# Performance work log

Measured on AMD Instinct MI355X. Metric: run time of the kernel, lower is better.

## Reference

```python
import jax, jax.numpy as jnp
import numpy as np

B, C, L = 8, 256, 2048
G = min(C // 4, 32)  # 32 groups
EPS = 1e-6


def group_norm(x, gamma, beta):
    # x: (B, C, L)
    xg = x.reshape(B, G, C // G, L)
    mean = xg.mean(axis=(2, 3), keepdims=True)
    var = xg.var(axis=(2, 3), keepdims=True)
    xn = ((xg - mean) * jax.lax.rsqrt(var + EPS)).reshape(B, C, L)
    return xn * gamma[None, :, None] + beta[None, :, None]


def nin(h, w, b):
    # 1x1 projection over channel dim: (B,C,L),(C,D)->(B,D,L)
    return jnp.einsum('bcl,cd->bdl', h, w) + b[None, :, None]


def setup_inputs() -> dict:
    key = jax.random.key(0)
    ks = jax.random.split(key, 10)
    s = 1.0 / np.sqrt(C)
    return {
        'x': jax.random.normal(ks[0], (B, C, L), dtype=jnp.float32),
        'gn_gamma': jnp.ones((C,), jnp.float32),
        'gn_beta': jnp.zeros((C,), jnp.float32),
        'w0': jax.random.normal(ks[1], (C, C), jnp.float32) * s,
        'b0': jnp.zeros((C,), jnp.float32),
        'w1': jax.random.normal(ks[2], (C, C), jnp.float32) * s,
        'b1': jnp.zeros((C,), jnp.float32),
        'w2': jax.random.normal(ks[3], (C, C), jnp.float32) * s,
        'b2': jnp.zeros((C,), jnp.float32),
        'w3': jax.random.normal(ks[4], (C, C), jnp.float32) * s,
        'b3': jnp.zeros((C,), jnp.float32),
    }


def reference(x, gn_gamma, gn_beta, w0, b0, w1, b1, w2, b2, w3, b3):
    h = group_norm(x, gn_gamma, gn_beta)
    q = nin(h, w0, b0)
    k = nin(h, w1, b1)
    v = nin(h, w2, b2)
    # attention scores over the L dim, scaled by 1/sqrt(C)
    w = jnp.einsum('bcl,bci->bli', q, k) * (C ** -0.5)  # (B, L, L)
    w = jax.nn.softmax(w, axis=-1)
    h = jnp.einsum('bli,bci->bcl', w, v)
    h = nin(h, w3, b3)
    return x + h  # skip_rescale=False
```

## Files before the change

### kernel.cpp

```cpp
#include <hip/hip_runtime.h>

#define B_ 8
#define C_ 256
#define L_ 2048
#define G_ 32
static constexpr long CL = (long)C_ * L_;
static constexpr long LL = (long)L_ * L_;

typedef __attribute__((ext_vector_type(8))) short bf16x8;
typedef __attribute__((ext_vector_type(4))) float f32x4;

__device__ __forceinline__ ushort f2bf(float f) {
    union { float f; unsigned u; } v; v.f = f;
    unsigned r = v.u + 0x7FFFu + ((v.u >> 16) & 1u);
    return (ushort)(r >> 16);
}
__device__ __forceinline__ float bf2f(ushort u) {
    union { unsigned u; float f; } v; v.u = (unsigned)u << 16;
    return v.f;
}

__device__ __forceinline__ void ld16(const ushort* g, ushort* l) {
    __builtin_amdgcn_global_load_lds(
        (const __attribute__((address_space(1))) unsigned int*)g,
        (__attribute__((address_space(3))) unsigned int*)l, 16, 0, 0);
}

__device__ __forceinline__ int swz8(int bid, int nwg) {
    return (bid & 7) * (nwg >> 3) + (bid >> 3);
}

template<int OP>
__device__ __forceinline__ float blockReduce(float v) {
    __shared__ float tmp[4];
    int lane = threadIdx.x & 63;
    int w    = threadIdx.x >> 6;
#pragma unroll
    for (int off = 32; off; off >>= 1) {
        float o = __shfl_down(v, off);
        v = OP ? fmaxf(v, o) : (v + o);
    }
    if (lane == 0) tmp[w] = v;
    __syncthreads();
    float r = OP ? fmaxf(fmaxf(tmp[0], tmp[1]), fmaxf(tmp[2], tmp[3]))
                 : (tmp[0] + tmp[1] + tmp[2] + tmp[3]);
    __syncthreads();
    return r;
}

__global__ __launch_bounds__(256) void gn_t_kernel(const float* __restrict__ x,
                                                   const float* __restrict__ gamma,
                                                   const float* __restrict__ beta,
                                                   ushort* __restrict__ hb) {
    int bg = blockIdx.x;
    int b  = bg >> 5, g = bg & 31;
    const float* xg = x + (long)bg * 16384;
    const float4* xv = (const float4*)xg;
    float s = 0.f, ss = 0.f;
    for (int i = threadIdx.x; i < 4096; i += 256) {
        float4 v = xv[i];
        s  += v.x + v.y + v.z + v.w;
        ss += v.x * v.x + v.y * v.y + v.z * v.z + v.w * v.w;
    }
    s  = blockReduce<0>(s);
    ss = blockReduce<0>(ss);
    float mean = s * (1.f / 16384.f);
    float var  = ss * (1.f / 16384.f) - mean * mean;
    float rstd = rsqrtf(var + 1e-6f);
    float a[8], bb[8];
#pragma unroll
    for (int cc = 0; cc < 8; ++cc) {
        int c = g * 8 + cc;
        a[cc]  = gamma[c] * rstd;
        bb[cc] = beta[c] - mean * a[cc];
    }
    ushort* hp = hb + (long)b * CL + g * 8;
    for (int l = threadIdx.x; l < 2048; l += 256) {
        ushort o[8];
#pragma unroll
        for (int cc = 0; cc < 8; ++cc)
            o[cc] = f2bf(xg[cc * 2048 + l] * a[cc] + bb[cc]);
        *(uint4*)&hp[(long)l * 256] = *(uint4*)o;
    }
}

__global__ void transpose_w(const float* __restrict__ w0, const float* __restrict__ w1,
                            const float* __restrict__ w2, const float* __restrict__ w3,
                            ushort* __restrict__ wT4) {
    int which = blockIdx.y;
    const float* w = which == 0 ? w0 : which == 1 ? w1 : which == 2 ? w2 : w3;
    int d = blockIdx.x, c = threadIdx.x;
    wT4[which * 65536 + d * 256 + c] = f2bf(w[c * 256 + d]);
}

template<int TM, int TN, int WR, int WC, bool DB>
__device__ __forceinline__ void gemm_body(const ushort* __restrict__ Mop,
                                          const ushort* __restrict__ Nop,
                                          long lda, long ldb, int K,
                                          ushort* As, ushort* Bs,
                                          f32x4 (&acc)[TM / (16 * WR)][TN / (16 * WC)]) {
    constexpr int NW = WR * WC;
    constexpr int CA = TM / (8 * NW), CB = TN / (8 * NW);
    constexpr int FM = TM / (16 * WR), FN = TN / (16 * WC);
    const int tid = threadIdx.x, lane = tid & 63, w = tid >> 6;
    const int r8 = lane >> 3, s8 = lane & 7;
    const int wrr = w / WC, wcc = w % WC;

    auto stage = [&](int buf, int k0) {
        ushort* Ad = As + buf * (TM * 64);
        ushort* Bd = Bs + buf * (TN * 64);
#pragma unroll
        for (int i = 0; i < CA; ++i) {
            int c = w * CA + i, row = c * 8 + r8;
            int ko = (s8 ^ (row & 7)) << 3;
            ld16(Mop + (long)row * lda + k0 + ko, Ad + c * 512);
        }
#pragma unroll
        for (int i = 0; i < CB; ++i) {
            int c = w * CB + i, row = c * 8 + r8;
            int ko = (s8 ^ (row & 7)) << 3;
            ld16(Nop + (long)row * ldb + k0 + ko, Bd + c * 512);
        }
    };

    auto compute = [&](int buf) {
        const ushort* Ac = As + buf * (TM * 64);
        const ushort* Bc = Bs + buf * (TN * 64);
#pragma unroll
        for (int kh = 0; kh < 2; ++kh) {
            int g = kh * 4 + (lane >> 4);
            bf16x8 av[FM], bv[FN];
#pragma unroll
            for (int mi = 0; mi < FM; ++mi) {
                int row = wrr * (TM / WR) + mi * 16 + (lane & 15);
                av[mi] = *(const bf16x8*)&Ac[row * 64 + ((g ^ (row & 7)) << 3)];
            }
#pragma unroll
            for (int ni = 0; ni < FN; ++ni) {
                int row = wcc * (TN / WC) + ni * 16 + (lane & 15);
                bv[ni] = *(const bf16x8*)&Bc[row * 64 + ((g ^ (row & 7)) << 3)];
            }
#pragma unroll
            for (int mi = 0; mi < FM; ++mi)
#pragma unroll
                for (int ni = 0; ni < FN; ++ni)
                    acc[mi][ni] = __builtin_amdgcn_mfma_f32_16x16x32_bf16(av[mi], bv[ni], acc[mi][ni], 0, 0, 0);
        }
    };

    if constexpr (!DB) {
        for (int k0 = 0; k0 < K; k0 += 64) {
            stage(0, k0);
            __syncthreads();
            compute(0);
            __syncthreads();
        }
    } else {
        stage(0, 0);
        asm volatile("s_waitcnt vmcnt(0)" ::: "memory");
        __builtin_amdgcn_s_barrier();
        int cur = 0;
        for (int k0 = 0; k0 < K; k0 += 64) {
            if (k0 + 64 < K) stage(cur ^ 1, k0 + 64);
            compute(cur);
            asm volatile("s_waitcnt vmcnt(0)" ::: "memory");
            __builtin_amdgcn_s_barrier();
            cur ^= 1;
        }
    }
}

#define GEMM_PROLOGUE(TM, TN, WR, WC, DBF)                    \
    __shared__ ushort As[DBF * TM * 64];                      \
    __shared__ ushort Bs[DBF * TN * 64];                      \
    f32x4 acc[TM / (16 * WR)][TN / (16 * WC)];                \
    _Pragma("unroll") for (int i = 0; i < TM / (16 * WR); ++i)     \
        _Pragma("unroll") for (int j = 0; j < TN / (16 * WC); ++j) \
            _Pragma("unroll") for (int e = 0; e < 4; ++e) acc[i][j][e] = 0.f; \
    const int lane = threadIdx.x & 63, wv = threadIdx.x >> 6; \
    const int wrr = wv / WC, wcc = wv % WC; (void)wrr; (void)wcc;

__global__ __launch_bounds__(256) void qkv_gemm(const ushort* __restrict__ wT4,
                                                const ushort* __restrict__ hb,
                                                ushort* __restrict__ qb,
                                                ushort* __restrict__ kb,
                                                ushort* __restrict__ vb,
                                                const float* __restrict__ bq,
                                                const float* __restrict__ bk,
                                                const float* __restrict__ bv_) {
    GEMM_PROLOGUE(128, 128, 2, 2, 1)
    int l = swz8(blockIdx.x, 768);
    int xn = l & 1, ym = (l >> 1) & 15, z = l >> 5;
    int which = z % 3, b = z / 3;
    int m0 = ym * 128, n0 = xn * 128;
    gemm_body<128, 128, 2, 2, false>(hb + (long)b * CL + (long)m0 * 256,
                                     wT4 + which * 65536 + (long)n0 * 256,
                                     256, 256, 256, As, Bs, acc);
    const float* bias = which == 0 ? bq : which == 1 ? bk : bv_;
    ushort* outp = (which == 0 ? qb : which == 1 ? kb : vb) + (long)b * CL;
#pragma unroll
    for (int mi = 0; mi < 4; ++mi) {
        int mb = m0 + wrr * 64 + mi * 16 + (lane >> 4) * 4;
#pragma unroll
        for (int ni = 0; ni < 4; ++ni) {
            int n = n0 + wcc * 64 + ni * 16 + (lane & 15);
            float bval = bias[n];
            if (which < 2) {
#pragma unroll
                for (int r = 0; r < 4; ++r)
                    outp[(long)(mb + r) * 256 + n] = f2bf(acc[mi][ni][r] + bval);
            } else {
                ushort o[4];
#pragma unroll
                for (int r = 0; r < 4; ++r) o[r] = f2bf(acc[mi][ni][r] + bval);
                *(ushort4*)&outp[(long)n * L_ + mb] = *(ushort4*)o;
            }
        }
    }
}

__global__ __launch_bounds__(512) void score_gemm(const ushort* __restrict__ qb,
                                                  const ushort* __restrict__ kb,
                                                  ushort* __restrict__ S,
                                                  float* __restrict__ rs) {
    GEMM_PROLOGUE(256, 128, 4, 2, 1)
    int l = swz8(blockIdx.x, 1024);
    int xn = l & 15, ym = (l >> 4) & 7, b = l >> 7;
    int m0 = ym * 256, n0 = xn * 128;
    gemm_body<256, 128, 4, 2, false>(qb + (long)b * CL + (long)m0 * 256,
                                     kb + (long)b * CL + (long)n0 * 256,
                                     256, 256, 256, As, Bs, acc);
    ushort* Sp = S + (long)b * LL;
    const int slot = xn * 2 + wcc;
#pragma unroll
    for (int mi = 0; mi < 4; ++mi) {
        int mb = m0 + wrr * 64 + mi * 16 + (lane >> 4) * 4;
#pragma unroll
        for (int r = 0; r < 4; ++r) {
            float psum = 0.f;
#pragma unroll
            for (int ni = 0; ni < 4; ++ni) {
                int n = n0 + wcc * 64 + ni * 16 + (lane & 15);
                float e = __expf(acc[mi][ni][r] * 0.0625f);
                ushort eb = f2bf(e);
                Sp[(long)(mb + r) * L_ + n] = eb;
                psum += bf2f(eb);
            }
#pragma unroll
            for (int off = 1; off <= 8; off <<= 1)
                psum += __shfl_xor(psum, off);
            if ((lane & 15) == 0)
                rs[((long)b * L_ + mb + r) * 32 + slot] = psum;
        }
    }
}

__global__ __launch_bounds__(256) void pv_gemm(const ushort* __restrict__ S,
                                               const ushort* __restrict__ vb,
                                               const float* __restrict__ rs,
                                               ushort* __restrict__ hh) {
    GEMM_PROLOGUE(64, 128, 2, 2, 2)
    int l = swz8(blockIdx.x, 512);
    int xn = l & 1, ym = (l >> 1) & 31, b = l >> 6;
    int m0 = ym * 64, n0 = xn * 128;
    gemm_body<64, 128, 2, 2, true>(S + (long)b * LL + (long)m0 * L_,
                                   vb + (long)b * CL + (long)n0 * L_,
                                   L_, L_, L_, As, Bs, acc);
    ushort* outp = hh + (long)b * CL;
#pragma unroll
    for (int mi = 0; mi < 2; ++mi) {
        int mb = m0 + wrr * 32 + mi * 16 + (lane >> 4) * 4;
        float rinv[4];
#pragma unroll
        for (int r = 0; r < 4; ++r) {
            const float4* rp = (const float4*)&rs[((long)b * L_ + mb + r) * 32];
            float4 s0 = rp[0], s1 = rp[1], s2 = rp[2], s3 = rp[3];
            float4 s4 = rp[4], s5 = rp[5], s6 = rp[6], s7 = rp[7];
            float t = s0.x + s0.y + s0.z + s0.w + s1.x + s1.y + s1.z + s1.w
                    + s2.x + s2.y + s2.z + s2.w + s3.x + s3.y + s3.z + s3.w
                    + s4.x + s4.y + s4.z + s4.w + s5.x + s5.y + s5.z + s5.w
                    + s6.x + s6.y + s6.z + s6.w + s7.x + s7.y + s7.z + s7.w;
            rinv[r] = 1.f / t;
        }
#pragma unroll
        for (int ni = 0; ni < 4; ++ni) {
            int n = n0 + wcc * 64 + ni * 16 + (lane & 15);
#pragma unroll
            for (int r = 0; r < 4; ++r)
                outp[(long)(mb + r) * 256 + n] = f2bf(acc[mi][ni][r] * rinv[r]);
        }
    }
}

__global__ __launch_bounds__(256) void final_gemm(const ushort* __restrict__ w3T,
                                                  const ushort* __restrict__ hh,
                                                  const float* __restrict__ x,
                                                  const float* __restrict__ b3,
                                                  float* __restrict__ outp) {
    GEMM_PROLOGUE(64, 128, 2, 2, 1)
    int l = swz8(blockIdx.x, 512);
    int xn = l & 15, ym = (l >> 4) & 3, b = l >> 6;
    int m0 = ym * 64, n0 = xn * 128;
    gemm_body<64, 128, 2, 2, false>(w3T + (long)m0 * 256,
                                    hh + (long)b * CL + (long)n0 * 256,
                                    256, 256, 256, As, Bs, acc);
    const float* xr = x + (long)b * CL;
    float* op = outp + (long)b * CL;
#pragma unroll
    for (int mi = 0; mi < 2; ++mi) {
        int mb = m0 + wrr * 32 + mi * 16 + (lane >> 4) * 4;
#pragma unroll
        for (int ni = 0; ni < 4; ++ni) {
            int n = n0 + wcc * 64 + ni * 16 + (lane & 15);
#pragma unroll
            for (int r = 0; r < 4; ++r) {
                long idx = (long)(mb + r) * L_ + n;
                op[idx] = acc[mi][ni][r] + b3[mb + r] + xr[idx];
            }
        }
    }
}

extern "C" void kernel_launch(void* const* d_in, const int* in_sizes, int n_in,
                              void* d_out, int out_size, void* d_ws, size_t ws_size,
                              hipStream_t stream) {
    const float* x     = (const float*)d_in[0];
    const float* gamma = (const float*)d_in[1];
    const float* beta  = (const float*)d_in[2];
    const float* w0 = (const float*)d_in[3];
    const float* b0 = (const float*)d_in[4];
    const float* w1 = (const float*)d_in[5];
    const float* b1 = (const float*)d_in[6];
    const float* w2 = (const float*)d_in[7];
    const float* b2 = (const float*)d_in[8];
    const float* w3 = (const float*)d_in[9];
    const float* b3 = (const float*)d_in[10];
    float* out = (float*)d_out;

    unsigned char* p = (unsigned char*)d_ws;
    ushort* hb = (ushort*)p; p += (size_t)B_ * CL * 2;
    ushort* qb = (ushort*)p; p += (size_t)B_ * CL * 2;
    ushort* kb = (ushort*)p; p += (size_t)B_ * CL * 2;
    ushort* vb = (ushort*)p; p += (size_t)B_ * CL * 2;
    ushort* S  = (ushort*)p; p += (size_t)B_ * LL * 2;
    float*  rs = (float*)p;  p += (size_t)B_ * L_ * 32 * 4;
    ushort* wT4 = (ushort*)p;
    ushort* hh = hb;

    transpose_w<<<dim3(256, 4), dim3(256), 0, stream>>>(w0, w1, w2, w3, wT4);
    gn_t_kernel<<<B_ * G_, dim3(256), 0, stream>>>(x, gamma, beta, hb);

    qkv_gemm<<<768, dim3(256), 0, stream>>>(wT4, hb, qb, kb, vb, b0, b1, b2);

    score_gemm<<<1024, dim3(512), 0, stream>>>(qb, kb, S, rs);

    pv_gemm<<<512, dim3(256), 0, stream>>>(S, vb, rs, hh);

    final_gemm<<<512, dim3(256), 0, stream>>>(wT4 + 3 * 65536, hh, x, b3, out);
}
```

Measured before the change: 203.3 us.

## Compute softmax row sums via MFMA in PV GEMM and retile score GEMM

Drops the partial row-sum buffer written by the score kernel. The PV GEMM now gets the softmax denominators from an extra MFMA that multiplies the S tile by a ones vector. The score GEMM is retiled from 256x128 blocks of 512 threads to 128x128 blocks of 256 threads with double buffering, and it uses exp2f with a pre-scaled constant plus paired bf16 conversion. This removes the shuffle reductions, the rs global traffic and its scattered loads, at the cost of extra MFMA work in the PV inner loop.

```diff
diff --git a/kernel.cpp b/kernel.cpp
--- a/kernel.cpp
+++ b/kernel.cpp
@@ -1,4 +1,5 @@
 #include <hip/hip_runtime.h>
+#include <hip/hip_bf16.h>
 
 #define B_ 8
 #define C_ 256
@@ -93,12 +94,13 @@
     wT4[which * 65536 + d * 256 + c] = f2bf(w[c * 256 + d]);
 }
 
-template<int TM, int TN, int WR, int WC, bool DB>
+template<int TM, int TN, int WR, int WC, bool DB, bool ROWSUM = false>
 __device__ __forceinline__ void gemm_body(const ushort* __restrict__ Mop,
                                           const ushort* __restrict__ Nop,
                                           long lda, long ldb, int K,
                                           ushort* As, ushort* Bs,
-                                          f32x4 (&acc)[TM / (16 * WR)][TN / (16 * WC)]) {
+                                          f32x4 (&acc)[TM / (16 * WR)][TN / (16 * WC)],
+                                          f32x4* rsacc = nullptr) {
     constexpr int NW = WR * WC;
     constexpr int CA = TM / (8 * NW), CB = TN / (8 * NW);
     constexpr int FM = TM / (16 * WR), FN = TN / (16 * WC);
@@ -106,6 +108,9 @@
     const int r8 = lane >> 3, s8 = lane & 7;
     const int wrr = w / WC, wcc = w % WC;
 
+    const short one_bf = (short)0x3F80;
+    bf16x8 ones = {one_bf, one_bf, one_bf, one_bf, one_bf, one_bf, one_bf, one_bf};
+
     auto stage = [&](int buf, int k0) {
         ushort* Ad = As + buf * (TM * 64);
         ushort* Bd = Bs + buf * (TN * 64);
@@ -139,6 +144,11 @@
             for (int ni = 0; ni < FN; ++ni) {
                 int row = wcc * (TN / WC) + ni * 16 + (lane & 15);
                 bv[ni] = *(const bf16x8*)&Bc[row * 64 + ((g ^ (row & 7)) << 3)];
+            }
+            if constexpr (ROWSUM) {
+#pragma unroll
+                for (int mi = 0; mi < FM; ++mi)
+                    rsacc[mi] = __builtin_amdgcn_mfma_f32_16x16x32_bf16(av[mi], ones, rsacc[mi], 0, 0, 0);
             }
 #pragma unroll
             for (int mi = 0; mi < FM; ++mi)
@@ -219,75 +229,75 @@
     }
 }
 
-__global__ __launch_bounds__(512) void score_gemm(const ushort* __restrict__ qb,
+__global__ __launch_bounds__(256) void score_gemm(const ushort* __restrict__ qb,
                                                   const ushort* __restrict__ kb,
-                                                  ushort* __restrict__ S,
-                                                  float* __restrict__ rs) {
-    GEMM_PROLOGUE(256, 128, 4, 2, 1)
-    int l = swz8(blockIdx.x, 1024);
-    int xn = l & 15, ym = (l >> 4) & 7, b = l >> 7;
-    int m0 = ym * 256, n0 = xn * 128;
-    gemm_body<256, 128, 4, 2, false>(qb + (long)b * CL + (long)m0 * 256,
-                                     kb + (long)b * CL + (long)n0 * 256,
-                                     256, 256, 256, As, Bs, acc);
+                                                  ushort* __restrict__ S) {
+    GEMM_PROLOGUE(128, 128, 2, 2, 2)
+    int l = swz8(blockIdx.x, 2048);
+    int xn = l & 15, ym = (l >> 4) & 15, b = l >> 8;
+    int m0 = ym * 128, n0 = xn * 128;
+    gemm_body<128, 128, 2, 2, true>(qb + (long)b * CL + (long)m0 * 256,
+                                    kb + (long)b * CL + (long)n0 * 256,
+                                    256, 256, 256, As, Bs, acc);
     ushort* Sp = S + (long)b * LL;
-    const int slot = xn * 2 + wcc;
+    const float SC = 0.09016994f;
 #pragma unroll
     for (int mi = 0; mi < 4; ++mi) {
         int mb = m0 + wrr * 64 + mi * 16 + (lane >> 4) * 4;
 #pragma unroll
-        for (int r = 0; r < 4; ++r) {
-            float psum = 0.f;
-#pragma unroll
-            for (int ni = 0; ni < 4; ++ni) {
-                int n = n0 + wcc * 64 + ni * 16 + (lane & 15);
-                float e = __expf(acc[mi][ni][r] * 0.0625f);
-                ushort eb = f2bf(e);
-                Sp[(long)(mb + r) * L_ + n] = eb;
-                psum += bf2f(eb);
-            }
-#pragma unroll
-            for (int off = 1; off <= 8; off <<= 1)
-                psum += __shfl_xor(psum, off);
-            if ((lane & 15) == 0)
-                rs[((long)b * L_ + mb + r) * 32 + slot] = psum;
+        for (int ni = 0; ni < 4; ++ni) {
+            int n = n0 + wcc * 64 + ni * 16 + (lane & 15);
+            float e0 = exp2f(acc[mi][ni][0] * SC);
+            float e1 = exp2f(acc[mi][ni][1] * SC);
+            float e2 = exp2f(acc[mi][ni][2] * SC);
+            float e3 = exp2f(acc[mi][ni][3] * SC);
+            union { __hip_bfloat162 h; ushort s[2]; } u0, u1;
+            u0.h = __float22bfloat162_rn(float2{e0, e1});
+            u1.h = __float22bfloat162_rn(float2{e2, e3});
+            long base = (long)mb * L_ + n;
+            Sp[base]          = u0.s[0];
+            Sp[base + L_]     = u0.s[1];
+            Sp[base + 2 * L_] = u1.s[0];
+            Sp[base + 3 * L_] = u1.s[1];
         }
     }
 }
 
 __global__ __launch_bounds__(256) void pv_gemm(const ushort* __restrict__ S,
                                                const ushort* __restrict__ vb,
-                                               const float* __restrict__ rs,
                                                ushort* __restrict__ hh) {
     GEMM_PROLOGUE(64, 128, 2, 2, 2)
+    f32x4 acc_rs[2];
+#pragma unroll
+    for (int i = 0; i < 2; ++i)
+#pragma unroll
+        for (int e = 0; e < 4; ++e) acc_rs[i][e] = 0.f;
     int l = swz8(blockIdx.x, 512);
     int xn = l & 1, ym = (l >> 1) & 31, b = l >> 6;
     int m0 = ym * 64, n0 = xn * 128;
-    gemm_body<64, 128, 2, 2, true>(S + (long)b * LL + (long)m0 * L_,
-                                   vb + (long)b * CL + (long)n0 * L_,
-                                   L_, L_, L_, As, Bs, acc);
+    gemm_body<64, 128, 2, 2, true, true>(S + (long)b * LL + (long)m0 * L_,
+                                         vb + (long)b * CL + (long)n0 * L_,
+                                         L_, L_, L_, As, Bs, acc, acc_rs);
     ushort* outp = hh + (long)b * CL;
 #pragma unroll
     for (int mi = 0; mi < 2; ++mi) {
         int mb = m0 + wrr * 32 + mi * 16 + (lane >> 4) * 4;
         float rinv[4];
 #pragma unroll
-        for (int r = 0; r < 4; ++r) {
-            const float4* rp = (const float4*)&rs[((long)b * L_ + mb + r) * 32];
-            float4 s0 = rp[0], s1 = rp[1], s2 = rp[2], s3 = rp[3];
-            float4 s4 = rp[4], s5 = rp[5], s6 = rp[6], s7 = rp[7];
-            float t = s0.x + s0.y + s0.z + s0.w + s1.x + s1.y + s1.z + s1.w
-                    + s2.x + s2.y + s2.z + s2.w + s3.x + s3.y + s3.z + s3.w
-                    + s4.x + s4.y + s4.z + s4.w + s5.x + s5.y + s5.z + s5.w
-                    + s6.x + s6.y + s6.z + s6.w + s7.x + s7.y + s7.z + s7.w;
-            rinv[r] = 1.f / t;
-        }
+        for (int r = 0; r < 4; ++r) rinv[r] = 1.f / acc_rs[mi][r];
 #pragma unroll
         for (int ni = 0; ni < 4; ++ni) {
             int n = n0 + wcc * 64 + ni * 16 + (lane & 15);
-#pragma unroll
-            for (int r = 0; r < 4; ++r)
-                outp[(long)(mb + r) * 256 + n] = f2bf(acc[mi][ni][r] * rinv[r]);
+            union { __hip_bfloat162 h; ushort s[2]; } u0, u1;
+            u0.h = __float22bfloat162_rn(float2{acc[mi][ni][0] * rinv[0],
+                                                acc[mi][ni][1] * rinv[1]});
+            u1.h = __float22bfloat162_rn(float2{acc[mi][ni][2] * rinv[2],
+                                                acc[mi][ni][3] * rinv[3]});
+            long base = (long)mb * 256 + n;
+            outp[base]       = u0.s[0];
+            outp[base + 256] = u0.s[1];
+            outp[base + 512] = u1.s[0];
+            outp[base + 768] = u1.s[1];
         }
     }
 }
@@ -343,7 +353,6 @@
     ushort* kb = (ushort*)p; p += (size_t)B_ * CL * 2;
     ushort* vb = (ushort*)p; p += (size_t)B_ * CL * 2;
     ushort* S  = (ushort*)p; p += (size_t)B_ * LL * 2;
-    float*  rs = (float*)p;  p += (size_t)B_ * L_ * 32 * 4;
     ushort* wT4 = (ushort*)p;
     ushort* hh = hb;
 
@@ -352,9 +361,9 @@
 
     qkv_gemm<<<768, dim3(256), 0, stream>>>(wT4, hb, qb, kb, vb, b0, b1, b2);
 
-    score_gemm<<<1024, dim3(512), 0, stream>>>(qb, kb, S, rs);
-
-    pv_gemm<<<512, dim3(256), 0, stream>>>(S, vb, rs, hh);
+    score_gemm<<<2048, dim3(256), 0, stream>>>(qb, kb, S);
+
+    pv_gemm<<<512, dim3(256), 0, stream>>>(S, vb, hh);
 
     final_gemm<<<512, dim3(256), 0, stream>>>(wT4 + 3 * 65536, hh, x, b3, out);
 }
```

Result: faster. 195.8 us (-3.7%).

## Fuse score and PV GEMMs into a flash-attention style kernel

Applied to the files above, without the earlier changes.

Replaces the separate score GEMM (which materialised exp scores and partial row sums in global memory) and the PV GEMM with a single kernel that computes QK^T per 64-key tile, exponentiates into LDS, and accumulates P·V and row sums via MFMA on chip. This removes the large L×L intermediate write and read. It trades that for a grid of only 256 large-LDS blocks with two barriers per step. The unused double-buffered GEMM path is dropped.

```diff
diff --git a/kernel.cpp b/kernel.cpp
--- a/kernel.cpp
+++ b/kernel.cpp
@@ -1,11 +1,11 @@
 #include <hip/hip_runtime.h>
+#include <hip/hip_bf16.h>
 
 #define B_ 8
 #define C_ 256
 #define L_ 2048
 #define G_ 32
 static constexpr long CL = (long)C_ * L_;
-static constexpr long LL = (long)L_ * L_;
 
 typedef __attribute__((ext_vector_type(8))) short bf16x8;
 typedef __attribute__((ext_vector_type(4))) float f32x4;
@@ -14,10 +14,6 @@
     union { float f; unsigned u; } v; v.f = f;
     unsigned r = v.u + 0x7FFFu + ((v.u >> 16) & 1u);
     return (ushort)(r >> 16);
-}
-__device__ __forceinline__ float bf2f(ushort u) {
-    union { unsigned u; float f; } v; v.u = (unsigned)u << 16;
-    return v.f;
 }
 
 __device__ __forceinline__ void ld16(const ushort* g, ushort* l) {
@@ -93,7 +89,7 @@
     wT4[which * 65536 + d * 256 + c] = f2bf(w[c * 256 + d]);
 }
 
-template<int TM, int TN, int WR, int WC, bool DB>
+template<int TM, int TN, int WR, int WC>
 __device__ __forceinline__ void gemm_body(const ushort* __restrict__ Mop,
                                           const ushort* __restrict__ Nop,
                                           long lda, long ldb, int K,
@@ -105,27 +101,20 @@
     const int tid = threadIdx.x, lane = tid & 63, w = tid >> 6;
     const int r8 = lane >> 3, s8 = lane & 7;
     const int wrr = w / WC, wcc = w % WC;
-
-    auto stage = [&](int buf, int k0) {
-        ushort* Ad = As + buf * (TM * 64);
-        ushort* Bd = Bs + buf * (TN * 64);
+    for (int k0 = 0; k0 < K; k0 += 64) {
 #pragma unroll
         for (int i = 0; i < CA; ++i) {
             int c = w * CA + i, row = c * 8 + r8;
             int ko = (s8 ^ (row & 7)) << 3;
-            ld16(Mop + (long)row * lda + k0 + ko, Ad + c * 512);
+            ld16(Mop + (long)row * lda + k0 + ko, As + c * 512);
         }
 #pragma unroll
         for (int i = 0; i < CB; ++i) {
             int c = w * CB + i, row = c * 8 + r8;
             int ko = (s8 ^ (row & 7)) << 3;
-            ld16(Nop + (long)row * ldb + k0 + ko, Bd + c * 512);
-        }
-    };
-
-    auto compute = [&](int buf) {
-        const ushort* Ac = As + buf * (TM * 64);
-        const ushort* Bc = Bs + buf * (TN * 64);
+            ld16(Nop + (long)row * ldb + k0 + ko, Bs + c * 512);
+        }
+        __syncthreads();
 #pragma unroll
         for (int kh = 0; kh < 2; ++kh) {
             int g = kh * 4 + (lane >> 4);
@@ -133,12 +122,12 @@
 #pragma unroll
             for (int mi = 0; mi < FM; ++mi) {
                 int row = wrr * (TM / WR) + mi * 16 + (lane & 15);
-                av[mi] = *(const bf16x8*)&Ac[row * 64 + ((g ^ (row & 7)) << 3)];
+                av[mi] = *(const bf16x8*)&As[row * 64 + ((g ^ (row & 7)) << 3)];
             }
 #pragma unroll
             for (int ni = 0; ni < FN; ++ni) {
                 int row = wcc * (TN / WC) + ni * 16 + (lane & 15);
-                bv[ni] = *(const bf16x8*)&Bc[row * 64 + ((g ^ (row & 7)) << 3)];
+                bv[ni] = *(const bf16x8*)&Bs[row * 64 + ((g ^ (row & 7)) << 3)];
             }
 #pragma unroll
             for (int mi = 0; mi < FM; ++mi)
@@ -146,33 +135,13 @@
                 for (int ni = 0; ni < FN; ++ni)
                     acc[mi][ni] = __builtin_amdgcn_mfma_f32_16x16x32_bf16(av[mi], bv[ni], acc[mi][ni], 0, 0, 0);
         }
-    };
-
-    if constexpr (!DB) {
-        for (int k0 = 0; k0 < K; k0 += 64) {
-            stage(0, k0);
-            __syncthreads();
-            compute(0);
-            __syncthreads();
-        }
-    } else {
-        stage(0, 0);
-        asm volatile("s_waitcnt vmcnt(0)" ::: "memory");
-        __builtin_amdgcn_s_barrier();
-        int cur = 0;
-        for (int k0 = 0; k0 < K; k0 += 64) {
-            if (k0 + 64 < K) stage(cur ^ 1, k0 + 64);
-            compute(cur);
-            asm volatile("s_waitcnt vmcnt(0)" ::: "memory");
-            __builtin_amdgcn_s_barrier();
-            cur ^= 1;
-        }
-    }
-}
-
-#define GEMM_PROLOGUE(TM, TN, WR, WC, DBF)                    \
-    __shared__ ushort As[DBF * TM * 64];                      \
-    __shared__ ushort Bs[DBF * TN * 64];                      \
+        __syncthreads();
+    }
+}
+
+#define GEMM_PROLOGUE(TM, TN, WR, WC)                         \
+    __shared__ ushort As[TM * 64];                            \
+    __shared__ ushort Bs[TN * 64];                            \
     f32x4 acc[TM / (16 * WR)][TN / (16 * WC)];                \
     _Pragma("unroll") for (int i = 0; i < TM / (16 * WR); ++i)     \
         _Pragma("unroll") for (int j = 0; j < TN / (16 * WC); ++j) \
@@ -188,14 +157,13 @@
                                                 const float* __restrict__ bq,
                                                 const float* __restrict__ bk,
                                                 const float* __restrict__ bv_) {
-    GEMM_PROLOGUE(128, 128, 2, 2, 1)
+    GEMM_PROLOGUE(128, 128, 2, 2)
     int l = swz8(blockIdx.x, 768);
     int xn = l & 1, ym = (l >> 1) & 15, z = l >> 5;
     int which = z % 3, b = z / 3;
     int m0 = ym * 128, n0 = xn * 128;
-    gemm_body<128, 128, 2, 2, false>(hb + (long)b * CL + (long)m0 * 256,
-                                     wT4 + which * 65536 + (long)n0 * 256,
-                                     256, 256, 256, As, Bs, acc);
+    gemm_body<128, 128, 2, 2>(hb + (long)b * CL + (long)m0 * 256,
+                              wT4 + which * 65536 + (long)n0 * 256, 256, 256, 256, As, Bs, acc);
     const float* bias = which == 0 ? bq : which == 1 ? bk : bv_;
     ushort* outp = (which == 0 ? qb : which == 1 ? kb : vb) + (long)b * CL;
 #pragma unroll
@@ -219,76 +187,134 @@
     }
 }
 
-__global__ __launch_bounds__(512) void score_gemm(const ushort* __restrict__ qb,
+__global__ __launch_bounds__(512) void flash_attn(const ushort* __restrict__ qb,
                                                   const ushort* __restrict__ kb,
-                                                  ushort* __restrict__ S,
-                                                  float* __restrict__ rs) {
-    GEMM_PROLOGUE(256, 128, 4, 2, 1)
-    int l = swz8(blockIdx.x, 1024);
-    int xn = l & 15, ym = (l >> 4) & 7, b = l >> 7;
-    int m0 = ym * 256, n0 = xn * 128;
-    gemm_body<256, 128, 4, 2, false>(qb + (long)b * CL + (long)m0 * 256,
-                                     kb + (long)b * CL + (long)n0 * 256,
-                                     256, 256, 256, As, Bs, acc);
-    ushort* Sp = S + (long)b * LL;
-    const int slot = xn * 2 + wcc;
-#pragma unroll
-    for (int mi = 0; mi < 4; ++mi) {
-        int mb = m0 + wrr * 64 + mi * 16 + (lane >> 4) * 4;
-#pragma unroll
-        for (int r = 0; r < 4; ++r) {
-            float psum = 0.f;
-#pragma unroll
-            for (int ni = 0; ni < 4; ++ni) {
-                int n = n0 + wcc * 64 + ni * 16 + (lane & 15);
-                float e = __expf(acc[mi][ni][r] * 0.0625f);
-                ushort eb = f2bf(e);
-                Sp[(long)(mb + r) * L_ + n] = eb;
-                psum += bf2f(eb);
-            }
-#pragma unroll
-            for (int off = 1; off <= 8; off <<= 1)
-                psum += __shfl_xor(psum, off);
-            if ((lane & 15) == 0)
-                rs[((long)b * L_ + mb + r) * 32 + slot] = psum;
-        }
-    }
-}
-
-__global__ __launch_bounds__(256) void pv_gemm(const ushort* __restrict__ S,
-                                               const ushort* __restrict__ vb,
-                                               const float* __restrict__ rs,
-                                               ushort* __restrict__ hh) {
-    GEMM_PROLOGUE(64, 128, 2, 2, 2)
-    int l = swz8(blockIdx.x, 512);
-    int xn = l & 1, ym = (l >> 1) & 31, b = l >> 6;
-    int m0 = ym * 64, n0 = xn * 128;
-    gemm_body<64, 128, 2, 2, true>(S + (long)b * LL + (long)m0 * L_,
-                                   vb + (long)b * CL + (long)n0 * L_,
-                                   L_, L_, L_, As, Bs, acc);
-    ushort* outp = hh + (long)b * CL;
-#pragma unroll
-    for (int mi = 0; mi < 2; ++mi) {
-        int mb = m0 + wrr * 32 + mi * 16 + (lane >> 4) * 4;
-        float rinv[4];
-#pragma unroll
-        for (int r = 0; r < 4; ++r) {
-            const float4* rp = (const float4*)&rs[((long)b * L_ + mb + r) * 32];
-            float4 s0 = rp[0], s1 = rp[1], s2 = rp[2], s3 = rp[3];
-            float4 s4 = rp[4], s5 = rp[5], s6 = rp[6], s7 = rp[7];
-            float t = s0.x + s0.y + s0.z + s0.w + s1.x + s1.y + s1.z + s1.w
-                    + s2.x + s2.y + s2.z + s2.w + s3.x + s3.y + s3.z + s3.w
-                    + s4.x + s4.y + s4.z + s4.w + s5.x + s5.y + s5.z + s5.w
-                    + s6.x + s6.y + s6.z + s6.w + s7.x + s7.y + s7.z + s7.w;
-            rinv[r] = 1.f / t;
-        }
-#pragma unroll
-        for (int ni = 0; ni < 4; ++ni) {
-            int n = n0 + wcc * 64 + ni * 16 + (lane & 15);
-#pragma unroll
-            for (int r = 0; r < 4; ++r)
-                outp[(long)(mb + r) * 256 + n] = f2bf(acc[mi][ni][r] * rinv[r]);
-        }
+                                                  const ushort* __restrict__ vb,
+                                                  ushort* __restrict__ hh) {
+    __shared__ ushort Qs[64 * 256];
+    __shared__ ushort Ks[2][64 * 256];
+    __shared__ ushort Vs[256 * 64];
+    __shared__ ushort Ps[64 * 64];
+
+    const int l = swz8(blockIdx.x, 256);
+    const int b = l >> 5, qt = l & 31;
+    const int q0 = qt * 64;
+    const ushort* qg = qb + (long)b * CL + (long)q0 * 256;
+    const ushort* kg = kb + (long)b * CL;
+    const ushort* vg = vb + (long)b * CL;
+
+    const int tid = threadIdx.x, lane = tid & 63, w = tid >> 6;
+    const int wr = w >> 2, wc = w & 3;
+    const int l15 = lane & 15, l4 = lane >> 4;
+
+    auto stage512 = [&](const ushort* src, ushort* dst) {
+#pragma unroll
+        for (int i = 0; i < 4; ++i) {
+            int blkI = w * 4 + i;
+            int row  = blkI * 2 + (lane >> 5);
+            int s    = (lane & 31) ^ (row & 7);
+            ld16(src + (long)row * 256 + s * 8, dst + blkI * 512);
+        }
+    };
+    auto stageV = [&](int kv0) {
+#pragma unroll
+        for (int i = 0; i < 4; ++i) {
+            int blkI = w * 4 + i;
+            int row  = blkI * 8 + (lane >> 3);
+            int s    = (lane & 7) ^ (row & 7);
+            ld16(vg + (long)row * L_ + kv0 + s * 8, Vs + blkI * 512);
+        }
+    };
+
+    f32x4 oacc[8];
+#pragma unroll
+    for (int i = 0; i < 8; ++i)
+#pragma unroll
+        for (int e = 0; e < 4; ++e) oacc[i][e] = 0.f;
+    f32x4 rsacc;
+#pragma unroll
+    for (int e = 0; e < 4; ++e) rsacc[e] = 0.f;
+
+    const short one_bf = (short)0x3F80;
+    const bf16x8 ones = {one_bf, one_bf, one_bf, one_bf, one_bf, one_bf, one_bf, one_bf};
+    const float SC = 0.09016844f;
+
+    stage512(qg, Qs);
+    stage512(kg, Ks[0]);
+    __syncthreads();
+
+    int cur = 0;
+#pragma unroll 1
+    for (int step = 0; step < 32; ++step) {
+        const int kv0 = step * 64;
+        stageV(kv0);
+        if (step + 1 < 32) stage512(kg + (long)(kv0 + 64) * 256, Ks[cur ^ 1]);
+
+        f32x4 sacc[2];
+#pragma unroll
+        for (int mi = 0; mi < 2; ++mi)
+#pragma unroll
+            for (int e = 0; e < 4; ++e) sacc[mi][e] = 0.f;
+        const ushort* Kc = Ks[cur];
+#pragma unroll
+        for (int kk = 0; kk < 8; ++kk) {
+            int g = kk * 4 + l4;
+            int qrow = wc * 16 + l15;
+            bf16x8 qv = *(const bf16x8*)&Qs[qrow * 256 + ((g ^ (qrow & 7)) << 3)];
+#pragma unroll
+            for (int mi = 0; mi < 2; ++mi) {
+                int krow = wr * 32 + mi * 16 + l15;
+                bf16x8 kvf = *(const bf16x8*)&Kc[krow * 256 + ((g ^ (krow & 7)) << 3)];
+                sacc[mi] = __builtin_amdgcn_mfma_f32_16x16x32_bf16(kvf, qv, sacc[mi], 0, 0, 0);
+            }
+        }
+        {
+            int q = wc * 16 + l15;
+#pragma unroll
+            for (int mi = 0; mi < 2; ++mi) {
+                float e0 = exp2f(sacc[mi][0] * SC);
+                float e1 = exp2f(sacc[mi][1] * SC);
+                float e2 = exp2f(sacc[mi][2] * SC);
+                float e3 = exp2f(sacc[mi][3] * SC);
+                union { __hip_bfloat162 h; uint u; } p0, p1;
+                p0.h = __float22bfloat162_rn(float2{e0, e1});
+                p1.h = __float22bfloat162_rn(float2{e2, e3});
+                int kvb = wr * 32 + mi * 16 + l4 * 4;
+                int off = q * 64 + (kvb ^ ((q & 7) << 3));
+                uint2 pk; pk.x = p0.u; pk.y = p1.u;
+                *(uint2*)&Ps[off] = pk;
+            }
+        }
+        __syncthreads();
+
+#pragma unroll
+        for (int kk2 = 0; kk2 < 2; ++kk2) {
+            int g2 = kk2 * 4 + l4;
+            int qrow = wc * 16 + l15;
+            bf16x8 pb = *(const bf16x8*)&Ps[qrow * 64 + ((g2 ^ (qrow & 7)) << 3)];
+            rsacc = __builtin_amdgcn_mfma_f32_16x16x32_bf16(ones, pb, rsacc, 0, 0, 0);
+#pragma unroll
+            for (int mi = 0; mi < 8; ++mi) {
+                int crow = wr * 128 + mi * 16 + l15;
+                bf16x8 av = *(const bf16x8*)&Vs[crow * 64 + ((g2 ^ (crow & 7)) << 3)];
+                oacc[mi] = __builtin_amdgcn_mfma_f32_16x16x32_bf16(av, pb, oacc[mi], 0, 0, 0);
+            }
+        }
+        __syncthreads();
+        cur ^= 1;
+    }
+
+    const float rinv = 1.f / rsacc[0];
+    const int q = wc * 16 + l15;
+    ushort* outp = hh + (long)b * CL + (long)(q0 + q) * 256;
+#pragma unroll
+    for (int mi = 0; mi < 8; ++mi) {
+        int c = wr * 128 + mi * 16 + l4 * 4;
+        union { __hip_bfloat162 h; uint u; } p0, p1;
+        p0.h = __float22bfloat162_rn(float2{oacc[mi][0] * rinv, oacc[mi][1] * rinv});
+        p1.h = __float22bfloat162_rn(float2{oacc[mi][2] * rinv, oacc[mi][3] * rinv});
+        uint2 pk; pk.x = p0.u; pk.y = p1.u;
+        *(uint2*)&outp[c] = pk;
     }
 }
 
@@ -297,13 +323,12 @@
                                                   const float* __restrict__ x,
                                                   const float* __restrict__ b3,
                                                   float* __restrict__ outp) {
-    GEMM_PROLOGUE(64, 128, 2, 2, 1)
+    GEMM_PROLOGUE(64, 128, 2, 2)
     int l = swz8(blockIdx.x, 512);
     int xn = l & 15, ym = (l >> 4) & 3, b = l >> 6;
     int m0 = ym * 64, n0 = xn * 128;
-    gemm_body<64, 128, 2, 2, false>(w3T + (long)m0 * 256,
-                                    hh + (long)b * CL + (long)n0 * 256,
-                                    256, 256, 256, As, Bs, acc);
+    gemm_body<64, 128, 2, 2>(w3T + (long)m0 * 256,
+                             hh + (long)b * CL + (long)n0 * 256, 256, 256, 256, As, Bs, acc);
     const float* xr = x + (long)b * CL;
     float* op = outp + (long)b * CL;
 #pragma unroll
@@ -342,8 +367,6 @@
     ushort* qb = (ushort*)p; p += (size_t)B_ * CL * 2;
     ushort* kb = (ushort*)p; p += (size_t)B_ * CL * 2;
     ushort* vb = (ushort*)p; p += (size_t)B_ * CL * 2;
-    ushort* S  = (ushort*)p; p += (size_t)B_ * LL * 2;
-    float*  rs = (float*)p;  p += (size_t)B_ * L_ * 32 * 4;
     ushort* wT4 = (ushort*)p;
     ushort* hh = hb;
 
@@ -352,9 +375,7 @@
 
     qkv_gemm<<<768, dim3(256), 0, stream>>>(wT4, hb, qb, kb, vb, b0, b1, b2);
 
-    score_gemm<<<1024, dim3(512), 0, stream>>>(qb, kb, S, rs);
-
-    pv_gemm<<<512, dim3(256), 0, stream>>>(S, vb, rs, hh);
+    flash_attn<<<256, dim3(512), 0, stream>>>(qb, kb, vb, hh);
 
     final_gemm<<<512, dim3(256), 0, stream>>>(wT4 + 3 * 65536, hh, x, b3, out);
 }
```

Measured after the change: 193.3 us. -4.9%, faster.
